# Kernel optimization log

Measured on AMD Instinct MI355X. Metric: run time of the kernel, lower is better.

Reference implementation:

```python
import jax, jax.numpy as jnp
import numpy as np
from jax import lax

B, D_IN, L = 32, 128, 2048
D_STATE = 512


def setup_inputs() -> dict:
    key = jax.random.key(0)
    ks = jax.random.split(key, 7)
    s_in = 1.0 / np.sqrt(D_STATE)
    return {
        "x": jax.random.normal(ks[0], (B, D_IN, L), dtype=jnp.float32),
        "W_ih": jax.random.normal(ks[1], (D_STATE, D_IN), dtype=jnp.float32) * s_in,
        "W_hh": jax.random.normal(ks[2], (D_STATE, D_STATE), dtype=jnp.float32) * s_in,
        "b_ih": jax.random.normal(ks[3], (D_STATE,), dtype=jnp.float32) * s_in,
        "b_hh": jax.random.normal(ks[4], (D_STATE,), dtype=jnp.float32) * s_in,
        "W_fc": jax.random.normal(ks[5], (D_IN, D_STATE), dtype=jnp.float32) * s_in,
        "b_fc": jax.random.normal(ks[6], (D_IN,), dtype=jnp.float32) * s_in,
    }


def reference(x, W_ih, W_hh, b_ih, b_hh, W_fc, b_fc):
    # x: [B, d_input, L] -> [L, B, d_input] (matches x.permute(2,0,1))
    xs = jnp.transpose(x, (2, 0, 1))
    L_, B_ = xs.shape[0], xs.shape[1]
    d_state = W_hh.shape[0]
    d_out = W_fc.shape[0]
    # precompute input projection for all timesteps: [L, B, d_state]
    pre = jnp.einsum('lbd,hd->lbh', xs, W_ih) + b_ih + b_hh

    def step(h, p):
        # h_t = tanh(W_ih x_t + b_ih + W_hh h_{t-1} + b_hh)
        h_new = jnp.tanh(p + h @ W_hh.T)
        return h_new, h_new

    h0 = jnp.zeros((B_, d_state), dtype=x.dtype)
    _, hs = lax.scan(step, h0, pre)  # hs: [L, B, d_state]

    h_flat = hs.reshape(-1, d_state)              # [L*B, d_state]
    y = jnp.tanh(h_flat @ W_fc.T + b_fc)          # [L*B, d_out]
    y = y.reshape(-1, d_out, L_)                  # matches torch reshape(-1, d_output, L)
    return y
```

## Files before the change

kernel.cpp:

```cpp
#include <hip/hip_runtime.h>
#include <cstdint>

typedef _Float16 half_t;
typedef __attribute__((ext_vector_type(2))) _Float16 half2_t;
typedef __attribute__((ext_vector_type(4))) _Float16 half4_t;
typedef __attribute__((ext_vector_type(8))) _Float16 half8_t;
typedef __attribute__((ext_vector_type(4))) float f32x4;

#define B_    32
#define DIN   128
#define LEN   2048
#define DS    512
#define NKT   16
#define KTR   12
#define KTL   (NKT - KTR)
#define LDSB_BYTES (KTL * 32 * 1024)
#define HBUF_OFF   LDSB_BYTES
#define LDS_BYTES  (LDSB_BYTES + 2 * DS * 2)

__device__ __forceinline__ float fast_tanh(float x) {
    float e = __expf(2.0f * x);
    return 1.0f - 2.0f / (e + 1.0f);
}

__device__ __forceinline__ float fd2(uint32_t a, uint32_t b, float c) {
    return __builtin_amdgcn_fdot2(__builtin_bit_cast(half2_t, a),
                                  __builtin_bit_cast(half2_t, b), c, false);
}

__device__ __forceinline__ half8_t load_wfrag(const float* __restrict__ W,
                                              int n0, int c, int q, int kt) {
    const float* p = W + (size_t)(n0 + c) * DS + kt * 32 + q * 8;
    float4 f0 = *(const float4*)p;
    float4 f1 = *(const float4*)(p + 4);
    half8_t r = {(half_t)f0.x, (half_t)f0.y, (half_t)f0.z, (half_t)f0.w,
                 (half_t)f1.x, (half_t)f1.y, (half_t)f1.z, (half_t)f1.w};
    return r;
}

__global__ __launch_bounds__(256) void rnn_pre_kernel(
    const float* __restrict__ x, const float* __restrict__ Wih,
    const float* __restrict__ bih, const float* __restrict__ bhh,
    half_t* __restrict__ pre)
{
    __shared__ half_t Xs[64 * 136];
    __shared__ half_t Ws[128 * 136];
    const int t  = threadIdx.x;
    const int l0 = blockIdx.x * 64;
    const int b  = blockIdx.y;
    const int h0 = blockIdx.z * 128;

#pragma unroll
    for (int i = 0; i < 32; ++i) {
        int idx = i * 256 + t;
        int j = idx & 63, d = idx >> 6;
        Xs[j * 136 + d] = (half_t)x[(size_t)b * DIN * LEN + (size_t)d * LEN + l0 + j];
    }
#pragma unroll
    for (int i = 0; i < 16; ++i) {
        int f4 = i * 256 + t;
        int h = f4 >> 5, d4 = f4 & 31;
        float4 w = *(const float4*)&Wih[(size_t)(h0 + h) * DIN + d4 * 4];
        half4_t hw = {(half_t)w.x, (half_t)w.y, (half_t)w.z, (half_t)w.w};
        *(half4_t*)&Ws[h * 136 + d4 * 4] = hw;
    }
    __syncthreads();

    const int lb = (t >> 4) * 4;
    const int hb = (t & 15) * 8;
    float acc[4][8];
#pragma unroll
    for (int i = 0; i < 4; ++i)
#pragma unroll
        for (int j = 0; j < 8; ++j) acc[i][j] = 0.f;

    for (int kc = 0; kc < DIN; kc += 8) {
        uint4 xa[4], wb[8];
#pragma unroll
        for (int i = 0; i < 4; ++i) xa[i] = *(const uint4*)&Xs[(lb + i) * 136 + kc];
#pragma unroll
        for (int j = 0; j < 8; ++j) wb[j] = *(const uint4*)&Ws[(hb + j) * 136 + kc];
#pragma unroll
        for (int i = 0; i < 4; ++i)
#pragma unroll
            for (int j = 0; j < 8; ++j) {
                float a = acc[i][j];
                a = fd2(xa[i].x, wb[j].x, a);
                a = fd2(xa[i].y, wb[j].y, a);
                a = fd2(xa[i].z, wb[j].z, a);
                a = fd2(xa[i].w, wb[j].w, a);
                acc[i][j] = a;
            }
    }

    float bias[8];
#pragma unroll
    for (int j = 0; j < 8; ++j) bias[j] = bih[h0 + hb + j] + bhh[h0 + hb + j];
#pragma unroll
    for (int i = 0; i < 4; ++i) {
        half8_t s;
#pragma unroll
        for (int j = 0; j < 8; ++j) s[j] = (half_t)(acc[i][j] + bias[j]);
        *(half8_t*)&pre[((size_t)b * LEN + l0 + lb + i) * DS + h0 + hb] = s;
    }
}

__global__ __launch_bounds__(512) __attribute__((amdgpu_waves_per_eu(2, 2)))
void rnn_recur_kernel(
    const float* __restrict__ Whh, const half_t* __restrict__ pre,
    half_t* __restrict__ hs)
{
    extern __shared__ char smem[];
    const int t    = threadIdx.x;
    const int b    = blockIdx.x;
    const int w    = t >> 6;
    const int lane = t & 63;
    const int c    = lane & 15;
    const int q    = lane >> 4;
    const int n0w  = w * 64;

    half8_t breg[KTR][4];
#pragma unroll
    for (int kt = 0; kt < KTR; ++kt)
#pragma unroll
        for (int nt = 0; nt < 4; ++nt)
            breg[kt][nt] = load_wfrag(Whh, n0w + nt * 16, c, q, kt);

#pragma unroll
    for (int kt = KTR; kt < NKT; ++kt)
#pragma unroll
        for (int nt = 0; nt < 4; ++nt) {
            half8_t f = load_wfrag(Whh, n0w + nt * 16, c, q, kt);
            int gid = w * 4 + nt;
            *(half8_t*)(smem + (((kt - KTR) * 32 + gid) << 10) + lane * 16) = f;
        }
    if (t < DS) *(half_t*)(smem + HBUF_OFF + t * 2) = (half_t)0.f;
    __syncthreads();

    const half_t* prew = pre + (size_t)b * LEN * DS + n0w + lane;
    half_t* hsb = hs + (size_t)b * DS;
    float pv_cur = (float)prew[0];

    int par = 0;
    for (int l = 0; l < LEN; ++l) {
        int ln = (l + 1 < LEN) ? (l + 1) : (LEN - 1);
        float pv_nxt = (float)prew[(size_t)ln * DS];

        const char* hb = smem + HBUF_OFF + par * 1024;
        f32x4 acc0 = {0.f, 0.f, 0.f, 0.f};
        f32x4 acc1 = {0.f, 0.f, 0.f, 0.f};
        f32x4 acc2 = {0.f, 0.f, 0.f, 0.f};
        f32x4 acc3 = {0.f, 0.f, 0.f, 0.f};
#pragma unroll
        for (int kt = 0; kt < KTR; ++kt) {
            half8_t a = *(const half8_t*)(hb + kt * 64 + q * 16);
            acc0 = __builtin_amdgcn_mfma_f32_16x16x32_f16(a, breg[kt][0], acc0, 0, 0, 0);
            acc1 = __builtin_amdgcn_mfma_f32_16x16x32_f16(a, breg[kt][1], acc1, 0, 0, 0);
            acc2 = __builtin_amdgcn_mfma_f32_16x16x32_f16(a, breg[kt][2], acc2, 0, 0, 0);
            acc3 = __builtin_amdgcn_mfma_f32_16x16x32_f16(a, breg[kt][3], acc3, 0, 0, 0);
        }
#pragma unroll
        for (int kt = KTR; kt < NKT; ++kt) {
            half8_t a = *(const half8_t*)(hb + kt * 64 + q * 16);
            const char* bb = smem + (((kt - KTR) * 32 + w * 4) << 10) + lane * 16;
            half8_t b0 = *(const half8_t*)(bb);
            half8_t b1 = *(const half8_t*)(bb + 1024);
            half8_t b2 = *(const half8_t*)(bb + 2048);
            half8_t b3 = *(const half8_t*)(bb + 3072);
            acc0 = __builtin_amdgcn_mfma_f32_16x16x32_f16(a, b0, acc0, 0, 0, 0);
            acc1 = __builtin_amdgcn_mfma_f32_16x16x32_f16(a, b1, acc1, 0, 0, 0);
            acc2 = __builtin_amdgcn_mfma_f32_16x16x32_f16(a, b2, acc2, 0, 0, 0);
            acc3 = __builtin_amdgcn_mfma_f32_16x16x32_f16(a, b3, acc3, 0, 0, 0);
        }

        float p0 = __shfl(pv_cur, c +  0, 64);
        float p1 = __shfl(pv_cur, c + 16, 64);
        float p2 = __shfl(pv_cur, c + 32, 64);
        float p3 = __shfl(pv_cur, c + 48, 64);

        if (q == 0) {
            half_t h0 = (half_t)fast_tanh(p0 + acc0.x);
            half_t h1 = (half_t)fast_tanh(p1 + acc1.x);
            half_t h2 = (half_t)fast_tanh(p2 + acc2.x);
            half_t h3 = (half_t)fast_tanh(p3 + acc3.x);
            char* hn = smem + HBUF_OFF + (par ^ 1) * 1024;
            *(half_t*)(hn + (n0w +  0 + c) * 2) = h0;
            *(half_t*)(hn + (n0w + 16 + c) * 2) = h1;
            *(half_t*)(hn + (n0w + 32 + c) * 2) = h2;
            *(half_t*)(hn + (n0w + 48 + c) * 2) = h3;
            half_t* hrow = hsb + (size_t)l * (B_ * DS);
            hrow[n0w +  0 + c] = h0;
            hrow[n0w + 16 + c] = h1;
            hrow[n0w + 32 + c] = h2;
            hrow[n0w + 48 + c] = h3;
        }
        pv_cur = pv_nxt;
        par ^= 1;
        __syncthreads();
    }
}

__global__ __launch_bounds__(256) void rnn_out_kernel(
    const half_t* __restrict__ hs, const float* __restrict__ Wfc,
    const float* __restrict__ bfc, float* __restrict__ y)
{
    __shared__ half_t Hs[64 * 72];
    __shared__ half_t Ws[128 * 72];
    const int t  = threadIdx.x;
    const int r0 = blockIdx.x * 64;

    const int lb = (t >> 4) * 4;
    const int ob = (t & 15) * 8;
    float acc[4][8];
#pragma unroll
    for (int i = 0; i < 4; ++i)
#pragma unroll
        for (int j = 0; j < 8; ++j) acc[i][j] = 0.f;

    for (int kc = 0; kc < DS; kc += 64) {
#pragma unroll
        for (int i = 0; i < 2; ++i) {
            int u = i * 256 + t;
            int r = u >> 3, c8 = u & 7;
            uint4 v = ((const uint4*)(hs + (size_t)(r0 + r) * DS + kc))[c8];
            *(uint4*)&Hs[r * 72 + c8 * 8] = v;
        }
#pragma unroll
        for (int i = 0; i < 8; ++i) {
            int u = i * 256 + t;
            int o = u >> 4, c4 = u & 15;
            float4 wv = *(const float4*)&Wfc[(size_t)o * DS + kc + c4 * 4];
            half4_t hw = {(half_t)wv.x, (half_t)wv.y, (half_t)wv.z, (half_t)wv.w};
            *(half4_t*)&Ws[o * 72 + c4 * 4] = hw;
        }
        __syncthreads();
#pragma unroll
        for (int k8 = 0; k8 < 64; k8 += 8) {
            uint4 xa[4], wb[8];
#pragma unroll
            for (int i = 0; i < 4; ++i) xa[i] = *(const uint4*)&Hs[(lb + i) * 72 + k8];
#pragma unroll
            for (int j = 0; j < 8; ++j) wb[j] = *(const uint4*)&Ws[(ob + j) * 72 + k8];
#pragma unroll
            for (int i = 0; i < 4; ++i)
#pragma unroll
                for (int j = 0; j < 8; ++j) {
                    float a = acc[i][j];
                    a = fd2(xa[i].x, wb[j].x, a);
                    a = fd2(xa[i].y, wb[j].y, a);
                    a = fd2(xa[i].z, wb[j].z, a);
                    a = fd2(xa[i].w, wb[j].w, a);
                    acc[i][j] = a;
                }
        }
        __syncthreads();
    }

#pragma unroll
    for (int i = 0; i < 4; ++i) {
        float4 r0v = {fast_tanh(acc[i][0] + bfc[ob + 0]), fast_tanh(acc[i][1] + bfc[ob + 1]),
                      fast_tanh(acc[i][2] + bfc[ob + 2]), fast_tanh(acc[i][3] + bfc[ob + 3])};
        float4 r1v = {fast_tanh(acc[i][4] + bfc[ob + 4]), fast_tanh(acc[i][5] + bfc[ob + 5]),
                      fast_tanh(acc[i][6] + bfc[ob + 6]), fast_tanh(acc[i][7] + bfc[ob + 7])};
        float* yr = y + (size_t)(r0 + lb + i) * DIN + ob;
        *(float4*)yr       = r0v;
        *((float4*)yr + 1) = r1v;
    }
}

extern "C" void kernel_launch(void* const* d_in, const int* in_sizes, int n_in,
                              void* d_out, int out_size, void* d_ws, size_t ws_size,
                              hipStream_t stream) {
    (void)in_sizes; (void)n_in; (void)out_size; (void)ws_size;
    const float* x   = (const float*)d_in[0];
    const float* Wih = (const float*)d_in[1];
    const float* Whh = (const float*)d_in[2];
    const float* bih = (const float*)d_in[3];
    const float* bhh = (const float*)d_in[4];
    const float* Wfc = (const float*)d_in[5];
    const float* bfc = (const float*)d_in[6];
    float* y = (float*)d_out;

    half_t* pre = (half_t*)d_ws;
    half_t* hs  = (half_t*)((char*)d_ws + (size_t)B_ * LEN * DS * 2);

    hipFuncSetAttribute((const void*)rnn_recur_kernel,
                        hipFuncAttributeMaxDynamicSharedMemorySize, LDS_BYTES);

    rnn_pre_kernel<<<dim3(LEN / 64, B_, DS / 128), 256, 0, stream>>>(x, Wih, bih, bhh, pre);
    rnn_recur_kernel<<<dim3(B_), 512, LDS_BYTES, stream>>>(Whh, pre, hs);
    rnn_out_kernel<<<dim3(LEN * B_ / 64), 256, 0, stream>>>(hs, Wfc, bfc, y);
}
```

Before: 3.369 ms.

## Stream part of recurrent weights from a pre-packed fp16 global buffer instead of LDS

Adds a small kernel that packs the tail k-tiles of W_hh into fp16 MFMA fragment order in workspace. The recurrence kernel keeps fewer k-tiles in registers and reloads the remaining six k-tiles every timestep from global memory (expected to stay L2-resident), double-buffered in registers, instead of reading them from LDS. The aim is to remove LDS bandwidth and latency from the serial per-step critical path and free register pressure. The cost is extra global/L2 traffic each step and more latency exposure; the old LDS path remains as a fallback when the workspace is too small.

```diff
diff --git a/kernel.cpp b/kernel.cpp
--- a/kernel.cpp
+++ b/kernel.cpp
@@ -12,11 +12,16 @@
 #define LEN   2048
 #define DS    512
 #define NKT   16
-#define KTR   12
-#define KTL   (NKT - KTR)
-#define LDSB_BYTES (KTL * 32 * 1024)
+
+#define KTR_S 10
+#define KTL_G (NKT - KTR_S)
+#define W16_BYTES (KTL_G * 32 * 1024)
+
+#define KTR_F 12
+#define KTL_F (NKT - KTR_F)
+#define LDSB_BYTES (KTL_F * 32 * 1024)
 #define HBUF_OFF   LDSB_BYTES
-#define LDS_BYTES  (LDSB_BYTES + 2 * DS * 2)
+#define LDSF_BYTES (LDSB_BYTES + 2 * DS * 2)
 
 __device__ __forceinline__ float fast_tanh(float x) {
     float e = __expf(2.0f * x);
@@ -36,6 +41,19 @@
     half8_t r = {(half_t)f0.x, (half_t)f0.y, (half_t)f0.z, (half_t)f0.w,
                  (half_t)f1.x, (half_t)f1.y, (half_t)f1.z, (half_t)f1.w};
     return r;
+}
+
+__global__ __launch_bounds__(64) void rnn_w16_kernel(
+    const float* __restrict__ Whh, half_t* __restrict__ W16)
+{
+    const int f    = blockIdx.x;
+    const int kt   = KTR_S + (f >> 5);
+    const int gid  = f & 31;
+    const int lane = threadIdx.x;
+    const int c    = lane & 15;
+    const int q    = lane >> 4;
+    half8_t w = load_wfrag(Whh, gid * 16, c, q, kt);
+    *(half8_t*)(W16 + (size_t)f * 512 + lane * 8) = w;
 }
 
 __global__ __launch_bounds__(256) void rnn_pre_kernel(
@@ -106,7 +124,102 @@
 }
 
 __global__ __launch_bounds__(512) __attribute__((amdgpu_waves_per_eu(2, 2)))
-void rnn_recur_kernel(
+void rnn_recur_stream(
+    const float* __restrict__ Whh, const half_t* __restrict__ W16,
+    const half_t* __restrict__ pre, half_t* __restrict__ hs)
+{
+    __shared__ half_t hbuf[2][DS];
+    const int t    = threadIdx.x;
+    const int b    = blockIdx.x;
+    const int w    = t >> 6;
+    const int lane = t & 63;
+    const int c    = lane & 15;
+    const int q    = lane >> 4;
+    const int n0w  = w * 64;
+
+    half8_t breg[KTR_S][4];
+#pragma unroll
+    for (int kt = 0; kt < KTR_S; ++kt)
+#pragma unroll
+        for (int nt = 0; nt < 4; ++nt)
+            breg[kt][nt] = load_wfrag(Whh, n0w + nt * 16, c, q, kt);
+
+    if (t < DS) hbuf[0][t] = (half_t)0.f;
+    __syncthreads();
+
+    const uint4* W16v = (const uint4*)W16 + ((w * 4) << 6) + lane;
+    const half_t* pp  = pre + (size_t)b * LEN * DS + n0w + c;
+    half_t* hsb = hs + (size_t)b * DS;
+
+    float pv_cur[4] = {0.f, 0.f, 0.f, 0.f};
+    if (q == 0) {
+#pragma unroll
+        for (int nt = 0; nt < 4; ++nt) pv_cur[nt] = (float)pp[nt * 16];
+    }
+
+    int par = 0;
+    for (int l = 0; l < LEN; ++l) {
+        const int ln = (l + 1 < LEN) ? (l + 1) : (LEN - 1);
+        float pv_nxt[4];
+        if (q == 0) {
+#pragma unroll
+            for (int nt = 0; nt < 4; ++nt)
+                pv_nxt[nt] = (float)pp[(size_t)ln * DS + nt * 16];
+        }
+
+        uint4 sb[2][4];
+#pragma unroll
+        for (int j = 0; j < 2; ++j)
+#pragma unroll
+            for (int nt = 0; nt < 4; ++nt)
+                sb[j][nt] = W16v[((j * 32 + nt) << 6)];
+
+        const char* hbp = (const char*)hbuf[par];
+        f32x4 acc[4];
+#pragma unroll
+        for (int nt = 0; nt < 4; ++nt) acc[nt] = (f32x4){0.f, 0.f, 0.f, 0.f};
+
+#pragma unroll
+        for (int kt = 0; kt < KTR_S; ++kt) {
+            half8_t a = *(const half8_t*)(hbp + kt * 64 + q * 16);
+#pragma unroll
+            for (int nt = 0; nt < 4; ++nt)
+                acc[nt] = __builtin_amdgcn_mfma_f32_16x16x32_f16(a, breg[kt][nt], acc[nt], 0, 0, 0);
+        }
+#pragma unroll
+        for (int kt = KTR_S; kt < NKT; ++kt) {
+            const int j = (kt - KTR_S) & 1;
+            half8_t a = *(const half8_t*)(hbp + kt * 64 + q * 16);
+#pragma unroll
+            for (int nt = 0; nt < 4; ++nt)
+                acc[nt] = __builtin_amdgcn_mfma_f32_16x16x32_f16(
+                    a, __builtin_bit_cast(half8_t, sb[j][nt]), acc[nt], 0, 0, 0);
+            if (kt + 2 < NKT) {
+#pragma unroll
+                for (int nt = 0; nt < 4; ++nt)
+                    sb[j][nt] = W16v[(((kt + 2 - KTR_S) * 32 + nt) << 6)];
+            }
+        }
+
+        if (q == 0) {
+            half_t* hn = hbuf[par ^ 1];
+            half_t* hrow = hsb + (size_t)l * (B_ * DS);
+#pragma unroll
+            for (int nt = 0; nt < 4; ++nt) {
+                half_t hv = (half_t)fast_tanh(pv_cur[nt] + acc[nt].x);
+                hn[n0w + nt * 16 + c] = hv;
+                hrow[n0w + nt * 16 + c] = hv;
+            }
+        }
+#pragma unroll
+        for (int nt = 0; nt < 4; ++nt) pv_cur[nt] = pv_nxt[nt];
+        par ^= 1;
+        __syncthreads();
+    }
+}
+
+__global__ __launch_bounds__(512) __attribute__((amdgpu_waves_per_eu(2, 2)))
+void rnn_recur_lds(
     const float* __restrict__ Whh, const half_t* __restrict__ pre,
     half_t* __restrict__ hs)
 {
@@ -119,20 +232,20 @@
     const int q    = lane >> 4;
     const int n0w  = w * 64;
 
-    half8_t breg[KTR][4];
-#pragma unroll
-    for (int kt = 0; kt < KTR; ++kt)
+    half8_t breg[KTR_F][4];
+#pragma unroll
+    for (int kt = 0; kt < KTR_F; ++kt)
 #pragma unroll
         for (int nt = 0; nt < 4; ++nt)
             breg[kt][nt] = load_wfrag(Whh, n0w + nt * 16, c, q, kt);
 
 #pragma unroll
-    for (int kt = KTR; kt < NKT; ++kt)
+    for (int kt = KTR_F; kt < NKT; ++kt)
 #pragma unroll
         for (int nt = 0; nt < 4; ++nt) {
             half8_t f = load_wfrag(Whh, n0w + nt * 16, c, q, kt);
             int gid = w * 4 + nt;
-            *(half8_t*)(smem + (((kt - KTR) * 32 + gid) << 10) + lane * 16) = f;
+            *(half8_t*)(smem + (((kt - KTR_F) * 32 + gid) << 10) + lane * 16) = f;
         }
     if (t < DS) *(half_t*)(smem + HBUF_OFF + t * 2) = (half_t)0.f;
     __syncthreads();
@@ -143,16 +256,14 @@
 
     int par = 0;
     for (int l = 0; l < LEN; ++l) {
-        int ln = (l + 1 < LEN) ? (l + 1) : (LEN - 1);
-        float pv_nxt = (float)prew[(size_t)ln * DS];
+        int lnx = (l + 1 < LEN) ? (l + 1) : (LEN - 1);
+        float pv_nxt = (float)prew[(size_t)lnx * DS];
 
         const char* hb = smem + HBUF_OFF + par * 1024;
-        f32x4 acc0 = {0.f, 0.f, 0.f, 0.f};
-        f32x4 acc1 = {0.f, 0.f, 0.f, 0.f};
-        f32x4 acc2 = {0.f, 0.f, 0.f, 0.f};
-        f32x4 acc3 = {0.f, 0.f, 0.f, 0.f};
-#pragma unroll
-        for (int kt = 0; kt < KTR; ++kt) {
+        f32x4 acc0 = {0.f,0.f,0.f,0.f}, acc1 = {0.f,0.f,0.f,0.f};
+        f32x4 acc2 = {0.f,0.f,0.f,0.f}, acc3 = {0.f,0.f,0.f,0.f};
+#pragma unroll
+        for (int kt = 0; kt < KTR_F; ++kt) {
             half8_t a = *(const half8_t*)(hb + kt * 64 + q * 16);
             acc0 = __builtin_amdgcn_mfma_f32_16x16x32_f16(a, breg[kt][0], acc0, 0, 0, 0);
             acc1 = __builtin_amdgcn_mfma_f32_16x16x32_f16(a, breg[kt][1], acc1, 0, 0, 0);
@@ -160,9 +271,9 @@
             acc3 = __builtin_amdgcn_mfma_f32_16x16x32_f16(a, breg[kt][3], acc3, 0, 0, 0);
         }
 #pragma unroll
-        for (int kt = KTR; kt < NKT; ++kt) {
+        for (int kt = KTR_F; kt < NKT; ++kt) {
             half8_t a = *(const half8_t*)(hb + kt * 64 + q * 16);
-            const char* bb = smem + (((kt - KTR) * 32 + w * 4) << 10) + lane * 16;
+            const char* bb = smem + (((kt - KTR_F) * 32 + w * 4) << 10) + lane * 16;
             half8_t b0 = *(const half8_t*)(bb);
             half8_t b1 = *(const half8_t*)(bb + 1024);
             half8_t b2 = *(const half8_t*)(bb + 2048);
@@ -271,7 +382,7 @@
 extern "C" void kernel_launch(void* const* d_in, const int* in_sizes, int n_in,
                               void* d_out, int out_size, void* d_ws, size_t ws_size,
                               hipStream_t stream) {
-    (void)in_sizes; (void)n_in; (void)out_size; (void)ws_size;
+    (void)in_sizes; (void)n_in; (void)out_size;
     const float* x   = (const float*)d_in[0];
     const float* Wih = (const float*)d_in[1];
     const float* Whh = (const float*)d_in[2];
@@ -281,13 +392,22 @@
     const float* bfc = (const float*)d_in[6];
     float* y = (float*)d_out;
 
+    const size_t preB = (size_t)B_ * LEN * DS * 2;
+    const size_t hsB  = (size_t)B_ * LEN * DS * 2;
     half_t* pre = (half_t*)d_ws;
-    half_t* hs  = (half_t*)((char*)d_ws + (size_t)B_ * LEN * DS * 2);
-
-    hipFuncSetAttribute((const void*)rnn_recur_kernel,
-                        hipFuncAttributeMaxDynamicSharedMemorySize, LDS_BYTES);
+    half_t* hs  = (half_t*)((char*)d_ws + preB);
+    half_t* W16 = (half_t*)((char*)d_ws + preB + hsB);
 
     rnn_pre_kernel<<<dim3(LEN / 64, B_, DS / 128), 256, 0, stream>>>(x, Wih, bih, bhh, pre);
-    rnn_recur_kernel<<<dim3(B_), 512, LDS_BYTES, stream>>>(Whh, pre, hs);
+
+    if (ws_size >= preB + hsB + W16_BYTES) {
+        rnn_w16_kernel<<<dim3(KTL_G * 32), 64, 0, stream>>>(Whh, W16);
+        rnn_recur_stream<<<dim3(B_), 512, 0, stream>>>(Whh, W16, pre, hs);
+    } else {
+        hipFuncSetAttribute((const void*)rnn_recur_lds,
+                            hipFuncAttributeMaxDynamicSharedMemorySize, LDSF_BYTES);
+        rnn_recur_lds<<<dim3(B_), 512, LDSF_BYTES, stream>>>(Whh, pre, hs);
+    }
+
     rnn_out_kernel<<<dim3(LEN * B_ / 64), 256, 0, stream>>>(hs, Wfc, bfc, y);
 }
```

Result: slower. 8.333 ms (+147.3%).
